# Performance work log

Hardware: AMD Instinct MI355X
Metric: run time of the kernel (lower is better)

## Reference

```python
import jax, jax.numpy as jnp
import numpy as np

N, E = 20000, 640000
ND, ED = 16, 8            # raw node/edge feature dims
H = 128                   # encoder hidden = gnn channels = mlp hidden
OUT = 2
L = 10                    # gnn layers (shared weights, per-layer layernorms)
NOISE_STD = 0.003
EPS = 1e-5


def _mlp(x, w1, b1, w2, b2):
    return jax.nn.relu(x @ w1 + b1) @ w2 + b2


def _ln(x, g, b):
    m = jnp.mean(x, axis=-1, keepdims=True)
    v = jnp.var(x, axis=-1, keepdims=True)
    return (x - m) * jax.lax.rsqrt(v + EPS) * g + b


def setup_inputs() -> dict:
    key = jax.random.key(0)
    ks = jax.random.split(key, 32)

    def w(k, i, o):
        return jax.random.normal(k, (i, o), jnp.float32) / np.sqrt(i)

    inp = {
        "x": jax.random.normal(ks[0], (N, ND), jnp.float32),
        "edge_attr": jax.random.normal(ks[1], (E, ED), jnp.float32),
        "edge_index": jax.random.randint(ks[2], (2, E), 0, N, jnp.int64),
        "node_noise": jax.random.normal(ks[3], (N, ND), jnp.float32) * NOISE_STD,
        "edge_noise": jax.random.normal(ks[4], (E, ED), jnp.float32) * NOISE_STD,
        # encoders
        "node_enc_w1": w(ks[5], ND, H), "node_enc_b1": jnp.zeros((H,), jnp.float32),
        "node_enc_w2": w(ks[6], H, H),  "node_enc_b2": jnp.zeros((H,), jnp.float32),
        "edge_enc_w1": w(ks[7], ED, H), "edge_enc_b1": jnp.zeros((H,), jnp.float32),
        "edge_enc_w2": w(ks[8], H, H),  "edge_enc_b2": jnp.zeros((H,), jnp.float32),
        # single shared MPNN (module instance reused across all L layers)
        "gnn_edge_w1": w(ks[9], 3 * H, H), "gnn_edge_b1": jnp.zeros((H,), jnp.float32),
        "gnn_edge_w2": w(ks[10], H, H),    "gnn_edge_b2": jnp.zeros((H,), jnp.float32),
        "gnn_node_w1": w(ks[11], 2 * H, H), "gnn_node_b1": jnp.zeros((H,), jnp.float32),
        "gnn_node_w2": w(ks[12], H, H),     "gnn_node_b2": jnp.zeros((H,), jnp.float32),
        # per-layer layernorms
        "x_ln_g": jnp.ones((L, H), jnp.float32), "x_ln_b": jnp.zeros((L, H), jnp.float32),
        "e_ln_g": jnp.ones((L, H), jnp.float32), "e_ln_b": jnp.zeros((L, H), jnp.float32),
        # decoder
        "dec_w1": w(ks[13], H, H),  "dec_b1": jnp.zeros((H,), jnp.float32),
        "dec_w2": w(ks[14], H, OUT), "dec_b2": jnp.zeros((OUT,), jnp.float32),
    }
    return inp


def reference(x, edge_attr, edge_index, node_noise, edge_noise,
              node_enc_w1, node_enc_b1, node_enc_w2, node_enc_b2,
              edge_enc_w1, edge_enc_b1, edge_enc_w2, edge_enc_b2,
              gnn_edge_w1, gnn_edge_b1, gnn_edge_w2, gnn_edge_b2,
              gnn_node_w1, gnn_node_b1, gnn_node_w2, gnn_node_b2,
              x_ln_g, x_ln_b, e_ln_g, e_ln_b,
              dec_w1, dec_b1, dec_w2, dec_b2):
    src = edge_index[0]  # x_j
    dst = edge_index[1]  # x_i (aggregation target)

    h = _mlp(x + node_noise, node_enc_w1, node_enc_b1, node_enc_w2, node_enc_b2)      # [N,H]
    e = _mlp(edge_attr + edge_noise, edge_enc_w1, edge_enc_b1, edge_enc_w2, edge_enc_b2)  # [E,H]

    for l in range(L):
        xi = h[dst]  # [E,H]
        xj = h[src]  # [E,H]
        # edge update: e + edge_mlp([x_i, x_j, e])
        e_new = e + _mlp(jnp.concatenate([xi, xj, e], axis=1),
                         gnn_edge_w1, gnn_edge_b1, gnn_edge_w2, gnn_edge_b2)
        # message: x_i + node_mlp([x_i, e_new]); aggr='add' over dst
        msg = xi + _mlp(jnp.concatenate([xi, e_new], axis=1),
                        gnn_node_w1, gnn_node_b1, gnn_node_w2, gnn_node_b2)
        h_agg = jax.ops.segment_sum(msg, dst, num_segments=N)
        h = _ln(h + h_agg, x_ln_g[l], x_ln_b[l])
        e = _ln(e + e_new, e_ln_g[l], e_ln_b[l])

    out = _mlp(h, dec_w1, dec_b1, dec_w2, dec_b2) - node_noise[:, :OUT]
    return out
```

## Files before the change

kernel.cpp:

```cpp
#include <hip/hip_runtime.h>
#include <stdio.h>

#define NN 20000
#define NE 640000
#define NL 10

typedef unsigned short u16;
typedef unsigned int u32;
typedef __attribute__((ext_vector_type(8))) __bf16 bf16x8;
typedef __attribute__((ext_vector_type(8))) unsigned short us8;
typedef __attribute__((ext_vector_type(4))) float f32x4;

__device__ __forceinline__ bf16x8 ldbf(const u16* p) {
  union { us8 u; bf16x8 b; } v;
  v.u = *(const us8*)p;
  return v.b;
}
__device__ __forceinline__ f32x4 zero4() {
  f32x4 z; z[0] = 0.f; z[1] = 0.f; z[2] = 0.f; z[3] = 0.f; return z;
}
__device__ __forceinline__ float bf2f(u16 u) {
  u32 x = ((u32)u) << 16;
  return __uint_as_float(x);
}
__device__ __forceinline__ u16 f2bf(float f) {
  u32 x = __float_as_uint(f);
  u32 r = (x + 0x7fffu + ((x >> 16) & 1u)) >> 16;
  return (u16)r;
}
__device__ __forceinline__ int lad(int row, int col) {
  return (row << 7) + ((((col >> 3) ^ (row & 15)) << 3) | (col & 7));
}
__device__ __forceinline__ uint2 pack4bf(const float f[4]) {
  uint2 u;
  u.x = (u32)f2bf(f[0]) | ((u32)f2bf(f[1]) << 16);
  u.y = (u32)f2bf(f[2]) | ((u32)f2bf(f[3]) << 16);
  return u;
}
__device__ __forceinline__ void unpack4bf(uint2 u, float f[4]) {
  f[0] = bf2f((u16)(u.x & 0xffffu)); f[1] = bf2f((u16)(u.x >> 16));
  f[2] = bf2f((u16)(u.y & 0xffffu)); f[3] = bf2f((u16)(u.y >> 16));
}

__global__ void LearnedSimModel_28716151341396_kernel() {}

__global__ void init_kernel(float* agg, int agg_n, int* cnt, int cnt_n) {
  int i = blockIdx.x * 256 + threadIdx.x;
  if (i < agg_n) agg[i] = 0.0f;
  if (i < cnt_n) cnt[i] = 0;
}

__global__ void idx_detect_kernel(const int* raw, int* flag) {
  if (threadIdx.x == 0 && blockIdx.x == 0) {
    int any = 0;
    for (int k = 0; k < 16; ++k) any = any | raw[2 * k + 1];
    flag[0] = (any != 0) ? 1 : 0;
  }
}

__global__ void idx_prep_kernel(const int* raw, const int* flag, int* idx0) {
  int i = blockIdx.x * 256 + threadIdx.x;
  if (i < 2 * NE) {
    int v;
    if (flag[0] != 0) v = raw[i];
    else v = (int)(((const long long*)raw)[i]);
    if (v < 0) v = 0;
    if (v >= NN) v = NN - 1;
    idx0[i] = v;
  }
}

__global__ void hist_kernel(const int* dst0, int* cnt) {
  int i = blockIdx.x * 256 + threadIdx.x;
  if (i < NE) atomicAdd(&cnt[dst0[i]], 1);
}

__global__ void prefix_kernel(const int* cnt, int* cursor) {
  __shared__ int buf[1024];
  __shared__ int carry;
  int t = threadIdx.x;
  if (t == 0) carry = 0;
  __syncthreads();
  for (int base = 0; base < NN; base += 1024) {
    int v = (base + t < NN) ? cnt[base + t] : 0;
    buf[t] = v;
    __syncthreads();
    for (int s = 1; s < 1024; s <<= 1) {
      int add = (t >= s) ? buf[t - s] : 0;
      __syncthreads();
      buf[t] += add;
      __syncthreads();
    }
    int excl = buf[t] - v + carry;
    if (base + t < NN) cursor[base + t] = excl;
    __syncthreads();
    if (t == 0) carry = carry + buf[1023];
    __syncthreads();
  }
}

__global__ void scatter_kernel(const int* src0, const int* dst0, int* cursor,
                               int* src_s, int* dst_s, int* perm) {
  int i = blockIdx.x * 256 + threadIdx.x;
  if (i < NE) {
    int d = dst0[i];
    int pos = atomicAdd(&cursor[d], 1);
    perm[pos] = i;
    src_s[pos] = src0[i];
    dst_s[pos] = d;
  }
}

__global__ void transpose_slice_kernel(const float* __restrict__ W,
                                       u16* __restrict__ Wt, int koff) {
  int i = blockIdx.x * 256 + threadIdx.x;
  int k = i >> 7, f = i & 127;
  Wt[f * 128 + k] = f2bf(W[(size_t)(koff + k) * 128 + f]);
}

__global__ void node_enc_kernel(const float* x, const float* noise,
                                const float* w1, const float* b1,
                                const float* w2, const float* b2,
                                float* h, u16* h16) {
  __shared__ float in16[16];
  __shared__ float t1s[128];
  int f = threadIdx.x;
  int n = blockIdx.x;
  if (f < 16) in16[f] = x[n * 16 + f] + noise[n * 16 + f];
  __syncthreads();
  float a = b1[f];
  for (int k = 0; k < 16; ++k) a += in16[k] * w1[k * 128 + f];
  t1s[f] = fmaxf(a, 0.0f);
  __syncthreads();
  float o = b2[f];
  for (int k = 0; k < 128; ++k) o += t1s[k] * w2[k * 128 + f];
  h[(long long)n * 128 + f] = o;
  h16[(long long)n * 128 + f] = f2bf(o);
}

__device__ __forceinline__ void gemm128(const u16* lds, const u16* Wt,
                                        int l16, int quad, int fb, f32x4 acc[2][4]) {
  for (int ks = 0; ks < 4; ++ks) {
    int kg = ks * 32 + quad * 8;
    bf16x8 b0 = ldbf(lds + lad(0 * 16 + l16, kg));
    bf16x8 b1 = ldbf(lds + lad(1 * 16 + l16, kg));
    bf16x8 b2 = ldbf(lds + lad(2 * 16 + l16, kg));
    bf16x8 b3 = ldbf(lds + lad(3 * 16 + l16, kg));
    for (int tt = 0; tt < 2; ++tt) {
      bf16x8 a = ldbf(Wt + (size_t)(fb + tt * 16 + l16) * 128 + kg);
      acc[tt][0] = __builtin_amdgcn_mfma_f32_16x16x32_bf16(a, b0, acc[tt][0], 0, 0, 0);
      acc[tt][1] = __builtin_amdgcn_mfma_f32_16x16x32_bf16(a, b1, acc[tt][1], 0, 0, 0);
      acc[tt][2] = __builtin_amdgcn_mfma_f32_16x16x32_bf16(a, b2, acc[tt][2], 0, 0, 0);
      acc[tt][3] = __builtin_amdgcn_mfma_f32_16x16x32_bf16(a, b3, acc[tt][3], 0, 0, 0);
    }
  }
}

__device__ __forceinline__ void gemm128x8(const u16* lds, const u16* Wt,
                                          int l16, int quad, int fb, f32x4 acc[8]) {
  for (int ks = 0; ks < 4; ++ks) {
    int kg = ks * 32 + quad * 8;
    bf16x8 a = ldbf(Wt + (size_t)(fb + l16) * 128 + kg);
#pragma unroll
    for (int et = 0; et < 8; ++et) {
      bf16x8 b = ldbf(lds + lad(et * 16 + l16, kg));
      acc[et] = __builtin_amdgcn_mfma_f32_16x16x32_bf16(a, b, acc[et], 0, 0, 0);
    }
  }
}

__global__ __launch_bounds__(256) void edge_enc_mfma(
    const float* __restrict__ attr, const float* __restrict__ noise,
    const int* __restrict__ perm,
    const float* __restrict__ w1, const float* __restrict__ b1,
    const u16* __restrict__ Wt2, const float* __restrict__ b2,
    u16* __restrict__ e)
{
  __shared__ __align__(16) u16 sT[64 * 128];
  __shared__ float sIn[64][8];
  __shared__ int sPerm[64];

  const int t = threadIdx.x;
  if (t < 64) sPerm[t] = perm[blockIdx.x * 64 + t];
  __syncthreads();

  for (int it = 0; it < 2; ++it) {
    int c = t + it * 256;
    int row = c >> 3, k = c & 7;
    int p = sPerm[row];
    sIn[row][k] = attr[(size_t)p * 8 + k] + noise[(size_t)p * 8 + k];
  }
  __syncthreads();

  {
    int f = t & 127;
    int r0 = (t >> 7) * 32;
    float wc[8];
    for (int k = 0; k < 8; ++k) wc[k] = w1[k * 128 + f];
    float bb = b1[f];
    for (int j = 0; j < 32; ++j) {
      int row = r0 + j;
      float a = bb;
      for (int k = 0; k < 8; ++k) a += sIn[row][k] * wc[k];
      sT[lad(row, f)] = f2bf(fmaxf(a, 0.f));
    }
  }
  __syncthreads();

  const int lane = t & 63;
  const int wave = t >> 6;
  const int l16 = lane & 15;
  const int quad = lane >> 4;
  const int fb = wave * 32;
  f32x4 acc[2][4];
  for (int tt = 0; tt < 2; ++tt)
    for (int et = 0; et < 4; ++et) acc[tt][et] = zero4();
  gemm128(sT, Wt2, l16, quad, fb, acc);
  u16* etile = e + (size_t)blockIdx.x * 8192;
  for (int tt = 0; tt < 2; ++tt) {
    int f0 = fb + tt * 16 + quad * 4;
    float4 bb = *(const float4*)(b2 + f0);
    float bbv[4] = {bb.x, bb.y, bb.z, bb.w};
    for (int et = 0; et < 4; ++et) {
      int row = et * 16 + l16;
      float o[4];
      for (int r = 0; r < 4; ++r) o[r] = acc[tt][et][r] + bbv[r];
      *(uint2*)(etile + lad(row, f0)) = pack4bf(o);
    }
  }
}

__global__ __launch_bounds__(256) void nprep_kernel(
    const u16* __restrict__ h16, const u16* __restrict__ Wt_np,
    float* __restrict__ nprep)
{
  __shared__ __align__(16) u16 sH[64 * 128];
  const int t = threadIdx.x;
  const int n0 = blockIdx.x * 64;

  for (int it = 0; it < 4; ++it) {
    int c = t + it * 256;
    int row = c >> 4, seg = c & 15;
    int n = n0 + row;
    if (n >= NN) n = NN - 1;
    us8 v = *(const us8*)(h16 + (size_t)n * 128 + seg * 8);
    *(us8*)(sH + ((row << 7) + ((seg ^ (row & 15)) << 3))) = v;
  }
  __syncthreads();

  const int lane = t & 63;
  const int wave = t >> 6;
  const int l16 = lane & 15;
  const int quad = lane >> 4;
  const int fb = wave * 96;
  f32x4 acc[6][4];
  for (int ft = 0; ft < 6; ++ft)
    for (int et = 0; et < 4; ++et) acc[ft][et] = zero4();
  for (int ks = 0; ks < 4; ++ks) {
    int kg = ks * 32 + quad * 8;
    bf16x8 b0 = ldbf(sH + lad(0 * 16 + l16, kg));
    bf16x8 b1 = ldbf(sH + lad(1 * 16 + l16, kg));
    bf16x8 b2 = ldbf(sH + lad(2 * 16 + l16, kg));
    bf16x8 b3 = ldbf(sH + lad(3 * 16 + l16, kg));
    for (int ft = 0; ft < 6; ++ft) {
      bf16x8 a = ldbf(Wt_np + (size_t)(fb + ft * 16 + l16) * 128 + kg);
      acc[ft][0] = __builtin_amdgcn_mfma_f32_16x16x32_bf16(a, b0, acc[ft][0], 0, 0, 0);
      acc[ft][1] = __builtin_amdgcn_mfma_f32_16x16x32_bf16(a, b1, acc[ft][1], 0, 0, 0);
      acc[ft][2] = __builtin_amdgcn_mfma_f32_16x16x32_bf16(a, b2, acc[ft][2], 0, 0, 0);
      acc[ft][3] = __builtin_amdgcn_mfma_f32_16x16x32_bf16(a, b3, acc[ft][3], 0, 0, 0);
    }
  }
  for (int ft = 0; ft < 6; ++ft) {
    int f0 = fb + ft * 16 + quad * 4;
    for (int et = 0; et < 4; ++et) {
      int n = n0 + et * 16 + l16;
      if (n < NN) *(f32x4*)(nprep + (size_t)n * 384 + f0) = acc[ft][et];
    }
  }
}

__global__ __launch_bounds__(512, 4) void gnn_edge_mfma(
    u16* __restrict__ eg,
    const int* __restrict__ src_s, const int* __restrict__ dst_s,
    const float* __restrict__ nprep,
    const u16* __restrict__ Wt_e1c, const float* __restrict__ be1,
    const u16* __restrict__ Wt_e2,  const float* __restrict__ be2,
    const u16* __restrict__ Wt_n1b, const float* __restrict__ bn1,
    const u16* __restrict__ Wt_n2,
    const float* __restrict__ lng, const float* __restrict__ lnb,
    float* __restrict__ agg)
{
  __shared__ __align__(16) char smem[74240];
  u16* sE = (u16*)smem;
  u16* sT = (u16*)(smem + 32768);
  float* msgf = (float*)smem;
  float* part_s = (float*)(smem + 65536);
  float* part_q = (float*)(smem + 69632);
  int* sDst = (int*)(smem + 73728);

  const int t = threadIdx.x;
  const int e0 = blockIdx.x * 128;
  const int lane = t & 63;
  const int wave = t >> 6;
  const int l16 = lane & 15;
  const int quad = lane >> 4;
  const int fb = wave * 16;
  const int f0 = fb + quad * 4;

  if (t < 128) sDst[t] = dst_s[e0 + t];

  int rd[8], rs[8];
#pragma unroll
  for (int et = 0; et < 8; ++et) {
    rd[et] = dst_s[e0 + et * 16 + l16];
    rs[et] = src_s[e0 + et * 16 + l16];
  }

  const u16* ebase = eg + (size_t)blockIdx.x * 16384;
#pragma unroll
  for (int it = 0; it < 4; ++it) {
    int c = it * 4096 + t * 8;
    *(us8*)(sE + c) = *(const us8*)(ebase + c);
  }
  __syncthreads();

  f32x4 acc[8];
#pragma unroll
  for (int et = 0; et < 8; ++et) acc[et] = zero4();
  gemm128x8(sE, Wt_e1c, l16, quad, fb, acc);
  {
    float4 bb = *(const float4*)(be1 + f0);
    float bbv[4] = {bb.x, bb.y, bb.z, bb.w};
#pragma unroll
    for (int et = 0; et < 8; ++et) {
      f32x4 av = *(const f32x4*)(nprep + (size_t)rd[et] * 384 + f0);
      f32x4 jv = *(const f32x4*)(nprep + (size_t)rs[et] * 384 + 128 + f0);
      int row = et * 16 + l16;
      float o[4];
      for (int r = 0; r < 4; ++r)
        o[r] = fmaxf(acc[et][r] + av[r] + jv[r] + bbv[r], 0.f);
      *(uint2*)(sT + lad(row, f0)) = pack4bf(o);
    }
  }
  __syncthreads();

#pragma unroll
  for (int et = 0; et < 8; ++et) acc[et] = zero4();
  gemm128x8(sT, Wt_e2, l16, quad, fb, acc);
  {
    float4 bb = *(const float4*)(be2 + f0);
    float bbv[4] = {bb.x, bb.y, bb.z, bb.w};
#pragma unroll
    for (int et = 0; et < 8; ++et) {
      int row = et * 16 + l16;
      float eo[4];
      unpack4bf(*(const uint2*)(sE + lad(row, f0)), eo);
      float en[4];
      for (int r = 0; r < 4; ++r) en[r] = eo[r] + acc[et][r] + bbv[r];
      *(uint2*)(sE + lad(row, f0)) = pack4bf(en);
      for (int r = 0; r < 4; ++r) acc[et][r] = eo[r] + en[r];
    }
  }
#pragma unroll
  for (int et = 0; et < 8; ++et) {
    float s = 0.f, q = 0.f;
    for (int r = 0; r < 4; ++r) {
      float v = acc[et][r];
      s += v; q += v * v;
    }
    s += __shfl_xor(s, 16); s += __shfl_xor(s, 32);
    q += __shfl_xor(q, 16); q += __shfl_xor(q, 32);
    if (quad == 0) {
      part_s[wave * 128 + et * 16 + l16] = s;
      part_q[wave * 128 + et * 16 + l16] = q;
    }
  }
  __syncthreads();

  u16* etile = eg + (size_t)blockIdx.x * 16384;
  {
    float4 g4 = *(const float4*)(lng + f0);
    float4 b4 = *(const float4*)(lnb + f0);
    float gv[4] = {g4.x, g4.y, g4.z, g4.w};
    float bv[4] = {b4.x, b4.y, b4.z, b4.w};
#pragma unroll
    for (int et = 0; et < 8; ++et) {
      int row = et * 16 + l16;
      float s = 0.f, q = 0.f;
      for (int w = 0; w < 8; ++w) {
        s += part_s[w * 128 + row];
        q += part_q[w * 128 + row];
      }
      float m = s * (1.f / 128.f);
      float var = q * (1.f / 128.f) - m * m;
      float rsv = rsqrtf(fmaxf(var, 0.f) + 1e-5f);
      float o[4];
      for (int r = 0; r < 4; ++r)
        o[r] = (acc[et][r] - m) * rsv * gv[r] + bv[r];
      *(uint2*)(etile + lad(row, f0)) = pack4bf(o);
    }
  }

#pragma unroll
  for (int et = 0; et < 8; ++et) acc[et] = zero4();
  gemm128x8(sE, Wt_n1b, l16, quad, fb, acc);
  {
    float4 bb = *(const float4*)(bn1 + f0);
    float bbv[4] = {bb.x, bb.y, bb.z, bb.w};
#pragma unroll
    for (int et = 0; et < 8; ++et) {
      f32x4 bv4 = *(const f32x4*)(nprep + (size_t)rd[et] * 384 + 256 + f0);
      int row = et * 16 + l16;
      float o[4];
      for (int r = 0; r < 4; ++r)
        o[r] = fmaxf(acc[et][r] + bv4[r] + bbv[r], 0.f);
      *(uint2*)(sT + lad(row, f0)) = pack4bf(o);
    }
  }
  __syncthreads();

#pragma unroll
  for (int et = 0; et < 8; ++et) acc[et] = zero4();
  gemm128x8(sT, Wt_n2, l16, quad, fb, acc);
  __syncthreads();

  {
    int c = f0 >> 2;
#pragma unroll
    for (int et = 0; et < 8; ++et) {
      int row = et * 16 + l16;
      *(f32x4*)(msgf + row * 128 + (((c ^ (row & 31)) & 31) << 2)) = acc[et];
    }
  }
  __syncthreads();

  {
    int f = t & 127, qtr = t >> 7;
    int c = f >> 2, c3 = f & 3;
    float a = 0.f;
    int j0 = qtr * 32;
    for (int j = j0; j < j0 + 32; ++j) {
      a += msgf[j * 128 + (((c ^ (j & 31)) & 31) << 2) + c3];
      int dj = sDst[j];
      if (j == j0 + 31 || sDst[j + 1] != dj) {
        atomicAdd(&agg[(size_t)dj * 128 + f], a);
        a = 0.f;
      }
    }
  }
}

__global__ void node_ln_kernel(float* h, u16* h16, float* agg,
                               const int* cnt, const float* bn2,
                               const float* g, const float* b) {
  __shared__ float red[128];
  int f = threadIdx.x;
  int n = blockIdx.x;
  long long base = (long long)n * 128 + f;
  float deg = (float)cnt[n];
  float hv = h[base];
  float v = hv + agg[base] + deg * (hv + bn2[f]);
  red[f] = v;
  __syncthreads();
  for (int s = 64; s > 0; s >>= 1) {
    if (f < s) red[f] += red[f + s];
    __syncthreads();
  }
  float m = red[0] * (1.0f / 128.0f);
  __syncthreads();
  red[f] = v * v;
  __syncthreads();
  for (int s = 64; s > 0; s >>= 1) {
    if (f < s) red[f] += red[f + s];
    __syncthreads();
  }
  float q = red[0] * (1.0f / 128.0f);
  float var = q - m * m;
  float rs = rsqrtf(fmaxf(var, 0.0f) + 1e-5f);
  float o = (v - m) * rs * g[f] + b[f];
  h[base] = o;
  h16[base] = f2bf(o);
  agg[base] = 0.0f;
}

__global__ void decoder_kernel(const float* h, const float* w1, const float* b1,
                               const float* w2, const float* b2,
                               const float* noise, float* out) {
  __shared__ float t1s[128];
  int f = threadIdx.x;
  int n = blockIdx.x;
  float a = b1[f];
  for (int k = 0; k < 128; ++k) a += h[(long long)n * 128 + k] * w1[k * 128 + f];
  t1s[f] = fmaxf(a, 0.0f);
  __syncthreads();
  if (f < 2) {
    float s = b2[f];
    for (int k = 0; k < 128; ++k) s += t1s[k] * w2[k * 2 + f];
    s -= noise[n * 16 + f];
    out[n * 2 + f] = s;
  }
}

extern "C" void kernel_launch(void* const* d_in, const int* in_sizes, int n_in,
                              void* d_out, int out_size, void* d_ws, size_t ws_size,
                              hipStream_t stream) {
  (void)in_sizes; (void)n_in; (void)out_size; (void)ws_size;

  const float* x      = (const float*)d_in[0];
  const float* eattr  = (const float*)d_in[1];
  const int*   eidx   = (const int*)d_in[2];
  const float* nnoise = (const float*)d_in[3];
  const float* enoise = (const float*)d_in[4];
  const float* ne_w1 = (const float*)d_in[5];  const float* ne_b1 = (const float*)d_in[6];
  const float* ne_w2 = (const float*)d_in[7];  const float* ne_b2 = (const float*)d_in[8];
  const float* ee_w1 = (const float*)d_in[9];  const float* ee_b1 = (const float*)d_in[10];
  const float* ee_w2 = (const float*)d_in[11]; const float* ee_b2 = (const float*)d_in[12];
  const float* ge_w1 = (const float*)d_in[13]; const float* ge_b1 = (const float*)d_in[14];
  const float* ge_w2 = (const float*)d_in[15]; const float* ge_b2 = (const float*)d_in[16];
  const float* gn_w1 = (const float*)d_in[17]; const float* gn_b1 = (const float*)d_in[18];
  const float* gn_w2 = (const float*)d_in[19]; const float* gn_b2 = (const float*)d_in[20];
  const float* xlng = (const float*)d_in[21]; const float* xlnb = (const float*)d_in[22];
  const float* elng = (const float*)d_in[23]; const float* elnb = (const float*)d_in[24];
  const float* d_w1 = (const float*)d_in[25]; const float* d_b1 = (const float*)d_in[26];
  const float* d_w2 = (const float*)d_in[27]; const float* d_b2 = (const float*)d_in[28];

  float* out = (float*)d_out;

  char* base = (char*)d_ws;
  size_t off = 0;
  int* idx0 = (int*)(base + off);    off += (size_t)2 * NE * 4;
  int* src_s = (int*)(base + off);   off += (size_t)NE * 4;
  int* dst_s = (int*)(base + off);   off += (size_t)NE * 4;
  int* perm = (int*)(base + off);    off += (size_t)NE * 4;
  int* cnt = (int*)(base + off);     off += (size_t)NN * 4;
  int* cursor = (int*)(base + off);  off += (size_t)NN * 4;
  int* flag = (int*)(base + off);    off += 16;
  float* h = (float*)(base + off);   off += (size_t)NN * 128 * 4;
  u16* h16 = (u16*)(base + off);     off += (size_t)NN * 128 * 2;
  float* agg = (float*)(base + off); off += (size_t)NN * 128 * 4;
  u16* e = (u16*)(base + off);       off += (size_t)NE * 128 * 2;
  float* nprep = (float*)(base + off); off += (size_t)NN * 384 * 4;
  u16* Wt_np = (u16*)(base + off);   off += (size_t)384 * 128 * 2;
  u16* Wt_e1c = (u16*)(base + off);  off += (size_t)128 * 128 * 2;
  u16* Wt_ge2 = (u16*)(base + off);  off += (size_t)128 * 128 * 2;
  u16* Wt_n1b = (u16*)(base + off);  off += (size_t)128 * 128 * 2;
  u16* Wt_gn2 = (u16*)(base + off);  off += (size_t)128 * 128 * 2;
  u16* Wt_ee2 = (u16*)(base + off);  off += (size_t)128 * 128 * 2;

  hipStreamCaptureStatus cs = hipStreamCaptureStatusNone;
  hipStreamIsCapturing(stream, &cs);
  const bool dbg = (cs == hipStreamCaptureStatusNone);

  const int* src0 = idx0;
  const int* dst0 = idx0 + NE;

  init_kernel<<<(NN * 128 + 255) / 256, 256, 0, stream>>>(agg, NN * 128, cnt, NN);
  idx_detect_kernel<<<1, 64, 0, stream>>>(eidx, flag);
  idx_prep_kernel<<<(2 * NE + 255) / 256, 256, 0, stream>>>(eidx, flag, idx0);

  hist_kernel<<<(NE + 255) / 256, 256, 0, stream>>>(dst0, cnt);
  prefix_kernel<<<1, 1024, 0, stream>>>(cnt, cursor);
  scatter_kernel<<<(NE + 255) / 256, 256, 0, stream>>>(src0, dst0, cursor,
                                                       src_s, dst_s, perm);

  transpose_slice_kernel<<<64, 256, 0, stream>>>(ge_w1, Wt_np, 0);
  transpose_slice_kernel<<<64, 256, 0, stream>>>(ge_w1, Wt_np + 16384, 128);
  transpose_slice_kernel<<<64, 256, 0, stream>>>(gn_w1, Wt_np + 32768, 0);
  transpose_slice_kernel<<<64, 256, 0, stream>>>(ge_w1, Wt_e1c, 256);
  transpose_slice_kernel<<<64, 256, 0, stream>>>(ge_w2, Wt_ge2, 0);
  transpose_slice_kernel<<<64, 256, 0, stream>>>(gn_w1, Wt_n1b, 128);
  transpose_slice_kernel<<<64, 256, 0, stream>>>(gn_w2, Wt_gn2, 0);
  transpose_slice_kernel<<<64, 256, 0, stream>>>(ee_w2, Wt_ee2, 0);

  node_enc_kernel<<<NN, 128, 0, stream>>>(x, nnoise, ne_w1, ne_b1, ne_w2, ne_b2, h, h16);
  edge_enc_mfma<<<NE / 64, 256, 0, stream>>>(eattr, enoise, perm,
                                             ee_w1, ee_b1, Wt_ee2, ee_b2, e);

  for (int l = 0; l < NL; ++l) {
    nprep_kernel<<<(NN + 63) / 64, 256, 0, stream>>>(h16, Wt_np, nprep);
    gnn_edge_mfma<<<NE / 128, 512, 0, stream>>>(e, src_s, dst_s, nprep,
        Wt_e1c, ge_b1, Wt_ge2, ge_b2, Wt_n1b, gn_b1, Wt_gn2,
        elng + l * 128, elnb + l * 128, agg);
    node_ln_kernel<<<NN, 128, 0, stream>>>(h, h16, agg, cnt, gn_b2,
                                           xlng + l * 128, xlnb + l * 128);
  }

  decoder_kernel<<<NN, 128, 0, stream>>>(h, d_w1, d_b1, d_w2, d_b2, nnoise, out);

  if (dbg) {
    hipStreamSynchronize(stream);
    float tbuf[6] = {0, 0, 0, 0, 0, 0};
    hipMemcpy(tbuf, h, 16, hipMemcpyDeviceToHost);
    hipMemcpy(tbuf + 4, out, 8, hipMemcpyDeviceToHost);
    fprintf(stderr, "KL r32 fat128: h[0..3]=%.5g %.5g %.5g %.5g out[0..1]=%.5g %.5g lasterr=%d\n",
            tbuf[0], tbuf[1], tbuf[2], tbuf[3], tbuf[4], tbuf[5], (int)hipGetLastError());
    fflush(stderr);
  }
}
```

Before: 3.181 ms.

## Fuse node layernorm into node-prep GEMM and skip final-layer edge write

Merges the per-node layernorm kernel with the node projection GEMM so the normalized h is converted to bf16 straight into LDS, removing the h16 buffer and one kernel launch per layer. It also skips the edge layernorm and writeback of e in the last layer, since the final e is never used. The cost is a heavier fused kernel with 64-row blocks replacing one-block-per-node LN, which changes the parallelism shape. It also adds mode flags that have to be sequenced correctly across layers.

```diff
diff --git a/kernel.cpp b/kernel.cpp
--- a/kernel.cpp
+++ b/kernel.cpp
@@ -121,7 +121,7 @@
 __global__ void node_enc_kernel(const float* x, const float* noise,
                                 const float* w1, const float* b1,
                                 const float* w2, const float* b2,
-                                float* h, u16* h16) {
+                                float* h) {
   __shared__ float in16[16];
   __shared__ float t1s[128];
   int f = threadIdx.x;
@@ -135,7 +135,6 @@
   float o = b2[f];
   for (int k = 0; k < 128; ++k) o += t1s[k] * w2[k * 128 + f];
   h[(long long)n * 128 + f] = o;
-  h16[(long long)n * 128 + f] = f2bf(o);
 }
 
 __device__ __forceinline__ void gemm128(const u16* lds, const u16* Wt,
@@ -230,21 +229,64 @@
   }
 }
 
-__global__ __launch_bounds__(256) void nprep_kernel(
-    const u16* __restrict__ h16, const u16* __restrict__ Wt_np,
-    float* __restrict__ nprep)
+__global__ __launch_bounds__(256) void node_ln_prep(
+    float* __restrict__ h, float* __restrict__ agg,
+    const int* __restrict__ cnt, const float* __restrict__ bn2,
+    const float* __restrict__ g, const float* __restrict__ b,
+    const u16* __restrict__ Wt_np, float* __restrict__ nprep, int mode)
 {
   __shared__ __align__(16) u16 sH[64 * 128];
   const int t = threadIdx.x;
   const int n0 = blockIdx.x * 64;
-
-  for (int it = 0; it < 4; ++it) {
-    int c = t + it * 256;
-    int row = c >> 4, seg = c & 15;
-    int n = n0 + row;
-    if (n >= NN) n = NN - 1;
-    us8 v = *(const us8*)(h16 + (size_t)n * 128 + seg * 8);
-    *(us8*)(sH + ((row << 7) + ((seg ^ (row & 15)) << 3))) = v;
+  const int row = t >> 2;
+  const int c0 = (t & 3) * 32;
+  int n = n0 + row;
+  const bool valid = n < NN;
+  const int nc = valid ? n : (NN - 1);
+
+  float v[32];
+  float* hp = h + (size_t)nc * 128 + c0;
+  if (mode & 1) {
+    float* ap = agg + (size_t)nc * 128 + c0;
+    float deg = (float)cnt[nc];
+    for (int k = 0; k < 32; k += 4) {
+      f32x4 hv = *(const f32x4*)(hp + k);
+      f32x4 av = *(const f32x4*)(ap + k);
+      f32x4 bb = *(const f32x4*)(bn2 + c0 + k);
+      for (int r = 0; r < 4; ++r) v[k + r] = hv[r] + av[r] + deg * (hv[r] + bb[r]);
+    }
+    float s = 0.f, q = 0.f;
+    for (int k = 0; k < 32; ++k) { s += v[k]; q += v[k] * v[k]; }
+    s += __shfl_xor(s, 1); s += __shfl_xor(s, 2);
+    q += __shfl_xor(q, 1); q += __shfl_xor(q, 2);
+    float m = s * (1.f / 128.f);
+    float var = q * (1.f / 128.f) - m * m;
+    float rs = rsqrtf(fmaxf(var, 0.f) + 1e-5f);
+    for (int k = 0; k < 32; k += 4) {
+      f32x4 g4 = *(const f32x4*)(g + c0 + k);
+      f32x4 b4 = *(const f32x4*)(b + c0 + k);
+      for (int r = 0; r < 4; ++r) v[k + r] = (v[k + r] - m) * rs * g4[r] + b4[r];
+    }
+    if (valid) {
+      for (int k = 0; k < 32; k += 4) {
+        f32x4 ov; for (int r = 0; r < 4; ++r) ov[r] = v[k + r];
+        *(f32x4*)(hp + k) = ov;
+        f32x4 z = zero4();
+        *(f32x4*)(ap + k) = z;
+      }
+    }
+  } else {
+    for (int k = 0; k < 32; k += 4) {
+      f32x4 hv = *(const f32x4*)(hp + k);
+      for (int r = 0; r < 4; ++r) v[k + r] = hv[r];
+    }
+  }
+  if (!(mode & 2)) return;
+
+  for (int k = 0; k < 32; k += 8) {
+    u16 tmp[8];
+    for (int r = 0; r < 8; ++r) tmp[r] = f2bf(v[k + r]);
+    *(uint4*)(sH + lad(row, c0 + k)) = *(const uint4*)tmp;
   }
   __syncthreads();
 
@@ -271,10 +313,10 @@
     }
   }
   for (int ft = 0; ft < 6; ++ft) {
-    int f0 = fb + ft * 16 + quad * 4;
+    int F = fb + ft * 16 + quad * 4;
     for (int et = 0; et < 4; ++et) {
-      int n = n0 + et * 16 + l16;
-      if (n < NN) *(f32x4*)(nprep + (size_t)n * 384 + f0) = acc[ft][et];
+      int n2 = n0 + et * 16 + l16;
+      if (n2 < NN) *(f32x4*)(nprep + (size_t)n2 * 384 + F) = acc[ft][et];
     }
   }
 }
@@ -288,7 +330,7 @@
     const u16* __restrict__ Wt_n1b, const float* __restrict__ bn1,
     const u16* __restrict__ Wt_n2,
     const float* __restrict__ lng, const float* __restrict__ lnb,
-    float* __restrict__ agg)
+    float* __restrict__ agg, int write_e)
 {
   __shared__ __align__(16) char smem[74240];
   u16* sE = (u16*)smem;
@@ -361,24 +403,26 @@
       for (int r = 0; r < 4; ++r) acc[et][r] = eo[r] + en[r];
     }
   }
-#pragma unroll
-  for (int et = 0; et < 8; ++et) {
-    float s = 0.f, q = 0.f;
-    for (int r = 0; r < 4; ++r) {
-      float v = acc[et][r];
-      s += v; q += v * v;
-    }
-    s += __shfl_xor(s, 16); s += __shfl_xor(s, 32);
-    q += __shfl_xor(q, 16); q += __shfl_xor(q, 32);
-    if (quad == 0) {
-      part_s[wave * 128 + et * 16 + l16] = s;
-      part_q[wave * 128 + et * 16 + l16] = q;
-    }
-  }
-  __syncthreads();
-
-  u16* etile = eg + (size_t)blockIdx.x * 16384;
-  {
+  if (write_e) {
+#pragma unroll
+    for (int et = 0; et < 8; ++et) {
+      float s = 0.f, q = 0.f;
+      for (int r = 0; r < 4; ++r) {
+        float v = acc[et][r];
+        s += v; q += v * v;
+      }
+      s += __shfl_xor(s, 16); s += __shfl_xor(s, 32);
+      q += __shfl_xor(q, 16); q += __shfl_xor(q, 32);
+      if (quad == 0) {
+        part_s[wave * 128 + et * 16 + l16] = s;
+        part_q[wave * 128 + et * 16 + l16] = q;
+      }
+    }
+  }
+  __syncthreads();
+
+  if (write_e) {
+    u16* etile = eg + (size_t)blockIdx.x * 16384;
     float4 g4 = *(const float4*)(lng + f0);
     float4 b4 = *(const float4*)(lnb + f0);
     float gv[4] = {g4.x, g4.y, g4.z, g4.w};
@@ -448,39 +492,6 @@
       }
     }
   }
-}
-
-__global__ void node_ln_kernel(float* h, u16* h16, float* agg,
-                               const int* cnt, const float* bn2,
-                               const float* g, const float* b) {
-  __shared__ float red[128];
-  int f = threadIdx.x;
-  int n = blockIdx.x;
-  long long base = (long long)n * 128 + f;
-  float deg = (float)cnt[n];
-  float hv = h[base];
-  float v = hv + agg[base] + deg * (hv + bn2[f]);
-  red[f] = v;
-  __syncthreads();
-  for (int s = 64; s > 0; s >>= 1) {
-    if (f < s) red[f] += red[f + s];
-    __syncthreads();
-  }
-  float m = red[0] * (1.0f / 128.0f);
-  __syncthreads();
-  red[f] = v * v;
-  __syncthreads();
-  for (int s = 64; s > 0; s >>= 1) {
-    if (f < s) red[f] += red[f + s];
-    __syncthreads();
-  }
-  float q = red[0] * (1.0f / 128.0f);
-  float var = q - m * m;
-  float rs = rsqrtf(fmaxf(var, 0.0f) + 1e-5f);
-  float o = (v - m) * rs * g[f] + b[f];
-  h[base] = o;
-  h16[base] = f2bf(o);
-  agg[base] = 0.0f;
 }
 
 __global__ void decoder_kernel(const float* h, const float* w1, const float* b1,
@@ -536,7 +547,6 @@
   int* cursor = (int*)(base + off);  off += (size_t)NN * 4;
   int* flag = (int*)(base + off);    off += 16;
   float* h = (float*)(base + off);   off += (size_t)NN * 128 * 4;
-  u16* h16 = (u16*)(base + off);     off += (size_t)NN * 128 * 2;
   float* agg = (float*)(base + off); off += (size_t)NN * 128 * 4;
   u16* e = (u16*)(base + off);       off += (size_t)NE * 128 * 2;
   float* nprep = (float*)(base + off); off += (size_t)NN * 384 * 4;
@@ -572,17 +582,21 @@
   transpose_slice_kernel<<<64, 256, 0, stream>>>(gn_w2, Wt_gn2, 0);
   transpose_slice_kernel<<<64, 256, 0, stream>>>(ee_w2, Wt_ee2, 0);
 
-  node_enc_kernel<<<NN, 128, 0, stream>>>(x, nnoise, ne_w1, ne_b1, ne_w2, ne_b2, h, h16);
+  node_enc_kernel<<<NN, 128, 0, stream>>>(x, nnoise, ne_w1, ne_b1, ne_w2, ne_b2, h);
   edge_enc_mfma<<<NE / 64, 256, 0, stream>>>(eattr, enoise, perm,
                                              ee_w1, ee_b1, Wt_ee2, ee_b2, e);
 
+  const int NB_N = (NN + 63) / 64;
+  node_ln_prep<<<NB_N, 256, 0, stream>>>(h, agg, cnt, gn_b2, xlng, xlnb,
+                                         Wt_np, nprep, 2);
+
   for (int l = 0; l < NL; ++l) {
-    nprep_kernel<<<(NN + 63) / 64, 256, 0, stream>>>(h16, Wt_np, nprep);
     gnn_edge_mfma<<<NE / 128, 512, 0, stream>>>(e, src_s, dst_s, nprep,
         Wt_e1c, ge_b1, Wt_ge2, ge_b2, Wt_n1b, gn_b1, Wt_gn2,
-        elng + l * 128, elnb + l * 128, agg);
-    node_ln_kernel<<<NN, 128, 0, stream>>>(h, h16, agg, cnt, gn_b2,
-                                           xlng + l * 128, xlnb + l * 128);
+        elng + l * 128, elnb + l * 128, agg, (l < NL - 1) ? 1 : 0);
+    node_ln_prep<<<NB_N, 256, 0, stream>>>(h, agg, cnt, gn_b2,
+        xlng + l * 128, xlnb + l * 128, Wt_np, nprep,
+        (l == NL - 1) ? 1 : 3);
   }
 
   decoder_kernel<<<NN, 128, 0, stream>>>(h, d_w1, d_b1, d_w2, d_b2, nnoise, out);
@@ -592,7 +606,7 @@
     float tbuf[6] = {0, 0, 0, 0, 0, 0};
     hipMemcpy(tbuf, h, 16, hipMemcpyDeviceToHost);
     hipMemcpy(tbuf + 4, out, 8, hipMemcpyDeviceToHost);
-    fprintf(stderr, "KL r32 fat128: h[0..3]=%.5g %.5g %.5g %.5g out[0..1]=%.5g %.5g lasterr=%d\n",
+    fprintf(stderr, "KL r33 fat128+fusedln+skipE: h[0..3]=%.5g %.5g %.5g %.5g out[0..1]=%.5g %.5g lasterr=%d\n",
             tbuf[0], tbuf[1], tbuf[2], tbuf[3], tbuf[4], tbuf[5], (int)hipGetLastError());
     fflush(stderr);
   }
```

New measurement: 3.208 ms. About the same (+0.8%).
